# Kernel optimization log

Hardware: AMD Instinct MI355X
Metric: run time of the kernel (lower is better)

Reference implementation:

```python
import jax, jax.numpy as jnp
import numpy as np

CUTOFF = 5.0
L_MAX = 3
N_MAX = 3
DEGREE = L_MAX * N_MAX
EPS = 1e-8
NUM_NODES = 50000
NUM_EDGES = 1000000
NUM_TRIPLETS = 8000000
F_NODE = 64
F_EDGE = 64

# spherical Bessel zeros z_{l,n} for l<3, n<3
SB_ZEROS = np.array([
    [3.141592653589793, 6.283185307179586, 9.42477796076938],
    [4.4934094579080615, 7.725251836938652, 10.904121659429897],
    [5.763459196895549, 9.09501133047736, 12.322940970567323],
], dtype=np.float32)


def cutoff_function(r, cutoff):
    ratio = r / cutoff
    return 1 - 6 * ratio**5 + 15 * ratio**4 - 10 * ratio**3


def legendre_all(x, l_max):
    # P_0..P_{l_max-1}(x), x = cos(angle); returns list of arrays like x
    out = [jnp.ones_like(x)]
    if l_max >= 2:
        out.append(x)
        for n in range(1, l_max - 1):
            out.append(((2 * n + 1) * x * out[n] - n * out[n - 1]) / (n + 1))
    return out


def spherical_bessel(x, order):
    # j_order(x) via upward recurrence, matching the torch small-x branches
    safe = jnp.where(x > EPS, x, 1.0)
    out = [jnp.where(x > EPS, jnp.sin(x) / safe, jnp.ones_like(x))]
    if order >= 1:
        out.append(jnp.where(x > EPS, (jnp.sin(x) / safe - jnp.cos(x)) / safe, x / 3))
        coeff = 3
        for n in range(1, order):
            coeff *= 2 * n + 3
            out.append(jnp.where(x > EPS, (2 * n + 1) / safe * out[n] - out[n - 1], x / coeff))
    return out[-1]


def setup_inputs() -> dict:
    key = jax.random.key(0)
    ks = jax.random.split(key, 12)
    edge_distances = jax.random.uniform(ks[0], (NUM_EDGES,), minval=0.5, maxval=CUTOFF, dtype=jnp.float32)
    triplet_angles = jax.random.uniform(ks[1], (NUM_TRIPLETS,), minval=-1.0, maxval=1.0, dtype=jnp.float32)  # cos values
    node_features = jax.random.normal(ks[2], (NUM_NODES, F_NODE), dtype=jnp.float32)
    edge_attr = jax.random.normal(ks[3], (NUM_EDGES, F_EDGE), dtype=jnp.float32)
    triplet_edge_index = jax.random.randint(ks[4], (2, NUM_TRIPLETS), 0, NUM_EDGES)
    edge_index = jax.random.randint(ks[5], (2, NUM_EDGES), 0, NUM_NODES)
    s1 = 1.0 / np.sqrt(F_NODE)
    W1 = jax.random.uniform(ks[6], (F_NODE, DEGREE), minval=-s1, maxval=s1, dtype=jnp.float32)
    b1 = jax.random.uniform(ks[7], (DEGREE,), minval=-s1, maxval=s1, dtype=jnp.float32)
    s2 = 1.0 / np.sqrt(DEGREE)
    Wm = jax.random.uniform(ks[8], (DEGREE, F_EDGE), minval=-s2, maxval=s2, dtype=jnp.float32)
    bm = jax.random.uniform(ks[9], (F_EDGE,), minval=-s2, maxval=s2, dtype=jnp.float32)
    Wg = jax.random.uniform(ks[10], (DEGREE, F_EDGE), minval=-s2, maxval=s2, dtype=jnp.float32)
    bg = jax.random.uniform(ks[11], (F_EDGE,), minval=-s2, maxval=s2, dtype=jnp.float32)
    return {
        'edge_distances': edge_distances, 'triplet_angles': triplet_angles,
        'node_features': node_features, 'edge_attr': edge_attr,
        'W1': W1, 'b1': b1, 'Wm': Wm, 'bm': bm, 'Wg': Wg, 'bg': bg,
        'triplet_edge_index': triplet_edge_index, 'edge_index': edge_index,
    }


def reference(edge_distances, triplet_angles, node_features, edge_attr,
              W1, b1, Wm, bm, Wg, bg, triplet_edge_index, edge_index):
    tij, tik = triplet_edge_index[0], triplet_edge_index[1]
    rij = edge_distances[tij]                      # [T]
    rik = edge_distances[tik]                      # [T]
    fc = cutoff_function(rij, CUTOFF) * cutoff_function(rik, CUTOFF)  # [T]

    # angular basis: sqrt((2l+1)/pi) * P_l(cos theta), [L, T]
    leg = legendre_all(triplet_angles, L_MAX)
    sph = jnp.stack([np.sqrt((2 * l + 1) / np.pi).astype(np.float32) * leg[l]
                     for l in range(L_MAX)])

    # radial basis: j_l(z_{l,n} * r_ik / cutoff), [L, N_MAX, T]
    zeros = jnp.asarray(SB_ZEROS)
    jnlk = jnp.stack([
        spherical_bessel(zeros[l][:, None] * rik[None, :] / CUTOFF, l)
        for l in range(L_MAX)
    ])

    # node gate: sigmoid(Linear(node_features)) -> [L, N_MAX, num_nodes]
    m = jax.nn.sigmoid(node_features @ W1 + b1)    # [num_nodes, DEGREE]
    m = m.T.reshape(L_MAX, N_MAX, -1)
    node_k = edge_index[1][tik]                    # [T]

    tmp = jnlk * sph[:, None, :] * fc[None, None, :] * m[:, :, node_k]  # [L, N_MAX, T]

    # scatter-sum triplets -> edges: [num_edges, DEGREE]
    mid = jax.ops.segment_sum(tmp.reshape(DEGREE, -1).T, tij, num_segments=NUM_EDGES)

    # GatedMLP: swish main branch * sigmoid gate branch
    edge_update = jax.nn.silu(mid @ Wm + bm) * jax.nn.sigmoid(mid @ Wg + bg)
    return edge_attr + edge_update
```

## Files before the change

### kernel.cpp

```cpp
#include <hip/hip_runtime.h>
#include <hip/hip_fp16.h>
#include <math.h>

#define CUTOFF_INV 0.2f
#define EPB_SHIFT 10
#define EPB 1024
#define HEPB 512
#define NBIN_MAX 1024
#define P1_CHUNK 4096
#define P1_THREADS 1024
#define P2_THREADS 512
#define SCAP 5120
#define GC_STRIDE 16

typedef unsigned int uint;
typedef unsigned short ushort;

__device__ __forceinline__ float fcut(float r) {
    float p = r * CUTOFF_INV;
    float p2 = p * p;
    float p3 = p2 * p;
    return 1.0f + p3 * (-10.0f + p * (15.0f - 6.0f * p));
}

__device__ __forceinline__ void legendre_s(float ca, float& s0, float& s1, float& s2) {
    s0 = 0.5641895835477563f;
    s1 = 0.9772050238058398f * ca;
    s2 = 1.2615662610100802f * (1.5f * ca * ca - 0.5f);
}

__device__ __forceinline__ void radial9(float rik, float* v) {
    float rr = rik * CUTOFF_INV;
    float inv = __builtin_amdgcn_rcpf(rr);
    inv = inv * (2.0f - rr * inv);
    float fcik = fcut(rik);

    const float Z0[3]  = {3.14159265358979324f, 6.28318530717958648f, 9.42477796076937972f};
    const float IZ0[3] = {1.0f / 3.14159265358979324f, 1.0f / 6.28318530717958648f, 1.0f / 9.42477796076937972f};
    const float Z1[3]  = {4.49340945790806150f, 7.72525183693865170f, 10.9041216594298970f};
    const float IZ1[3] = {1.0f / 4.49340945790806150f, 1.0f / 7.72525183693865170f, 1.0f / 10.9041216594298970f};
    const float Z2[3]  = {5.76345919689554900f, 9.09501133047736000f, 12.3229409705673230f};
    const float IZ2[3] = {1.0f / 5.76345919689554900f, 1.0f / 9.09501133047736000f, 1.0f / 12.3229409705673230f};

#pragma unroll
    for (int n = 0; n < 3; ++n) {
        float x = Z0[n] * rr;
        float invx = IZ0[n] * inv;
        v[n] = __sinf(x) * invx * fcik;
    }
#pragma unroll
    for (int n = 0; n < 3; ++n) {
        float x = Z1[n] * rr;
        float invx = IZ1[n] * inv;
        float s, c;
        __sincosf(x, &s, &c);
        v[3 + n] = (s * invx - c) * invx * fcik;
    }
#pragma unroll
    for (int n = 0; n < 3; ++n) {
        float x = Z2[n] * rr;
        float invx = IZ2[n] * inv;
        float s, c;
        __sincosf(x, &s, &c);
        float sx = s * invx;
        float j1 = (sx - c) * invx;
        v[6 + n] = (3.0f * invx * j1 - sx) * fcik;
    }
}

__device__ __forceinline__ float h2f(uint w) { return __half2float(__ushort_as_half((ushort)w)); }

__device__ __forceinline__ void contrib9(uint2 r, const uint* __restrict__ gate16h, float* c) {
    uint nk = r.y & 0xFFFFu;
    const uint* G = gate16h + ((size_t)nk << 3);
    uint4 q = *(const uint4*)G;
    uint q8 = G[4];
    float ca  = h2f(r.x >> 16);
    float rik = h2f(r.x & 0xFFFFu);
    float vr[9];
    radial9(rik, vr);
    float s0, s1, s2;
    legendre_s(ca, s0, s1, s2);
    c[0] = vr[0] * h2f(q.x & 0xFFFFu) * s0;
    c[1] = vr[1] * h2f(q.x >> 16) * s0;
    c[2] = vr[2] * h2f(q.y & 0xFFFFu) * s0;
    c[3] = vr[3] * h2f(q.y >> 16) * s1;
    c[4] = vr[4] * h2f(q.z & 0xFFFFu) * s1;
    c[5] = vr[5] * h2f(q.z >> 16) * s1;
    c[6] = vr[6] * h2f(q.w & 0xFFFFu) * s2;
    c[7] = vr[7] * h2f(q.w >> 16) * s2;
    c[8] = vr[8] * h2f(q8 & 0xFFFFu) * s2;
}

__global__ void node_gate_h16_kernel(const float* __restrict__ nf,
                                     const float* __restrict__ W1,
                                     const float* __restrict__ b1,
                                     uint* __restrict__ gate16h, int N) {
    __shared__ float sW[64 * 9];
    __shared__ float sb[9];
    for (int i = threadIdx.x; i < 576; i += blockDim.x) sW[i] = W1[i];
    if (threadIdx.x < 9) sb[threadIdx.x] = b1[threadIdx.x];
    __syncthreads();
    int t = blockIdx.x * blockDim.x + threadIdx.x;
    if (t >= N) return;
    float acc[9];
#pragma unroll
    for (int d = 0; d < 9; ++d) acc[d] = sb[d];
    const float* row = nf + (size_t)t * 64;
#pragma unroll
    for (int f = 0; f < 64; ++f) {
        float x = row[f];
#pragma unroll
        for (int d = 0; d < 9; ++d) acc[d] += x * sW[f * 9 + d];
    }
    float g[9];
#pragma unroll
    for (int d = 0; d < 9; ++d) g[d] = 1.0f / (1.0f + __expf(-acc[d]));
    uint* o = gate16h + ((size_t)t << 3);
#pragma unroll
    for (int d = 0; d < 4; ++d) {
        uint lo = (uint)__half_as_ushort(__float2half_rn(g[2 * d]));
        uint hi = (uint)__half_as_ushort(__float2half_rn(g[2 * d + 1]));
        o[d] = lo | (hi << 16);
    }
    o[4] = (uint)__half_as_ushort(__float2half_rn(g[8]));
    o[5] = 0u; o[6] = 0u; o[7] = 0u;
}

__global__ void node_gate_f32_kernel(const float* __restrict__ nf,
                                     const float* __restrict__ W1,
                                     const float* __restrict__ b1,
                                     float* __restrict__ gate, int N) {
    __shared__ float sW[64 * 9];
    __shared__ float sb[9];
    for (int i = threadIdx.x; i < 576; i += blockDim.x) sW[i] = W1[i];
    if (threadIdx.x < 9) sb[threadIdx.x] = b1[threadIdx.x];
    __syncthreads();
    int t = blockIdx.x * blockDim.x + threadIdx.x;
    if (t >= N) return;
    float acc[9];
#pragma unroll
    for (int d = 0; d < 9; ++d) acc[d] = sb[d];
    const float* row = nf + (size_t)t * 64;
#pragma unroll
    for (int f = 0; f < 64; ++f) {
        float x = row[f];
#pragma unroll
        for (int d = 0; d < 9; ++d) acc[d] += x * sW[f * 9 + d];
    }
#pragma unroll
    for (int d = 0; d < 9; ++d)
        gate[(size_t)t * 9 + d] = 1.0f / (1.0f + __expf(-acc[d]));
}

__global__ void edge_tab_kernel(const float* __restrict__ dist,
                                const int* __restrict__ eidx,
                                uint* __restrict__ tab, int E) {
    int e = blockIdx.x * blockDim.x + threadIdx.x;
    if (e >= E) return;
    uint rh = (uint)__half_as_ushort(__float2half_rn(dist[e]));
    tab[e] = (rh << 16) | (uint)eidx[E + e];
}

__device__ __forceinline__ void spill_rec(uint2 rec, int bin,
                                          const uint* __restrict__ gate16h,
                                          float* __restrict__ mid) {
    float c[9];
    contrib9(rec, gate16h, c);
    uint ijl = rec.y >> 16;
    float* dst = mid + ((size_t)bin * EPB + ijl) * 9;
#pragma unroll
    for (int d = 0; d < 9; ++d) atomicAdd(dst + d, c[d]);
}

__global__ void __launch_bounds__(P1_THREADS) p1_sort_kernel(
        const float* __restrict__ ang,
        const int* __restrict__ tidx,
        const uint* __restrict__ tab,
        uint* __restrict__ gcount,
        uint2* __restrict__ binbuf,
        const uint* __restrict__ gate16h,
        float* __restrict__ mid,
        int T, int NBIN, int BCAP) {
    __shared__ uint hist[NBIN_MAX];
    __shared__ uint sc[NBIN_MAX];
    __shared__ uint gbase[NBIN_MAX];
    __shared__ uint lcur[NBIN_MAX];
    __shared__ uint2 sbuf[P1_CHUNK];
    __shared__ ushort sbin[P1_CHUNK];

    int t0 = blockIdx.x * P1_CHUNK;
    int m = T - t0;
    if (m <= 0) return;
    if (m > P1_CHUNK) m = P1_CHUNK;
    int tid = threadIdx.x;

    for (int i = tid; i < NBIN; i += blockDim.x) { hist[i] = 0; lcur[i] = 0; }
    __syncthreads();

    for (int i = tid; i < m; i += blockDim.x)
        atomicAdd(&hist[((uint)tidx[t0 + i]) >> EPB_SHIFT], 1u);
    __syncthreads();

    if (tid < NBIN) sc[tid] = hist[tid];
    __syncthreads();
    for (int off = 1; off < NBIN; off <<= 1) {
        uint v = 0;
        if (tid < NBIN) {
            v = sc[tid];
            if (tid >= off) v += sc[tid - off];
        }
        __syncthreads();
        if (tid < NBIN) sc[tid] = v;
        __syncthreads();
    }
    uint ex = 0, h = 0;
    if (tid < NBIN) {
        h = hist[tid];
        ex = sc[tid] - h;
    }
    __syncthreads();
    if (tid < NBIN) {
        sc[tid] = ex;
        gbase[tid] = h ? atomicAdd(&gcount[tid * GC_STRIDE], h) : 0u;
    }
    __syncthreads();

    for (int i = tid; i < m; i += blockDim.x) {
        int t = t0 + i;
        uint ij = (uint)tidx[t];
        uint ik = (uint)tidx[T + t];
        float ca = ang[t];
        uint te = tab[ik];
        uint bin = ij >> EPB_SHIFT;
        uint loc = atomicAdd(&lcur[bin], 1u);
        uint p = sc[bin] + loc;
        uint cah = (uint)__half_as_ushort(__float2half_rn(ca));
        sbuf[p] = make_uint2((cah << 16) | (te >> 16),
                             ((ij & (EPB - 1u)) << 16) | (te & 0xFFFFu));
        sbin[p] = (ushort)bin;
    }
    __syncthreads();

    for (int i = tid; i < m; i += blockDim.x) {
        uint bin = sbin[i];
        uint2 rec = sbuf[i];
        uint slot = gbase[bin] + ((uint)i - sc[bin]);
        if (slot < (uint)BCAP) {
            binbuf[(size_t)bin * BCAP + slot] = rec;
        } else {
            atomicOr(&gcount[bin * GC_STRIDE + 1], 1u);
            spill_rec(rec, bin, gate16h, mid);
        }
    }
}

__global__ void __launch_bounds__(P2_THREADS) p2_sorted_kernel(
        const float* __restrict__ dist,
        const uint* __restrict__ gate16h,
        const uint* __restrict__ gcount,
        const uint2* __restrict__ binbuf,
        const float* __restrict__ mid,
        const float* __restrict__ attr,
        const float* __restrict__ Wm,
        const float* __restrict__ bm,
        const float* __restrict__ Wg,
        const float* __restrict__ bg,
        float* __restrict__ out,
        int E, int BCAP) {
    __shared__ uint2 srec[SCAP];
    __shared__ uint cnt[HEPB];
    __shared__ uint off[HEPB];
    __shared__ float sWm[576], sWg[576], sbm[64], sbg[64];
    float* umid = (float*)srec;

    int tid = threadIdx.x;
    for (int i = tid; i < 576; i += P2_THREADS) { sWm[i] = Wm[i]; sWg[i] = Wg[i]; }
    if (tid < 64) { sbm[tid] = bm[tid]; sbg[tid] = bg[tid]; }
    cnt[tid] = 0;

    int bin = blockIdx.x >> 1;
    int hh  = blockIdx.x & 1;
    int ebase = (bin << EPB_SHIFT) + hh * HEPB;
    int ecnt = E - ebase; if (ecnt < 0) ecnt = 0; if (ecnt > HEPB) ecnt = HEPB;

    uint n = gcount[bin * GC_STRIDE];
    uint has_spill = gcount[bin * GC_STRIDE + 1];
    if (n > (uint)BCAP) n = (uint)BCAP;
    const uint2* rb = binbuf + (size_t)bin * BCAP;
    __syncthreads();

    for (uint i = tid; i < n; i += P2_THREADS) {
        uint ijl = rb[i].y >> 16;
        if ((ijl >> 9) == (uint)hh) atomicAdd(&cnt[ijl & (HEPB - 1u)], 1u);
    }
    __syncthreads();
    uint myCnt = cnt[tid];
    off[tid] = myCnt;
    __syncthreads();
    for (int o = 1; o < HEPB; o <<= 1) {
        uint add = (tid >= o) ? off[tid - o] : 0u;
        __syncthreads();
        off[tid] += add;
        __syncthreads();
    }
    uint total = off[HEPB - 1];
    uint myBase = off[tid] - myCnt;
    __syncthreads();
    off[tid] = myBase;
    cnt[tid] = 0;
    __syncthreads();

    float acc[9];
#pragma unroll
    for (int d = 0; d < 9; ++d) acc[d] = 0.0f;

    if (total <= (uint)SCAP) {
        for (uint i = tid; i < n; i += P2_THREADS) {
            uint2 r = rb[i];
            uint ijl = r.y >> 16;
            if ((ijl >> 9) == (uint)hh) {
                uint e = ijl & (HEPB - 1u);
                uint p = off[e] + atomicAdd(&cnt[e], 1u);
                srec[p] = r;
            }
        }
        __syncthreads();
        for (uint j = 0; j < myCnt; ++j) {
            float c[9];
            contrib9(srec[myBase + j], gate16h, c);
#pragma unroll
            for (int d = 0; d < 9; ++d) acc[d] += c[d];
        }
        __syncthreads();
    } else {
        for (int i = tid; i < HEPB * 9; i += P2_THREADS) umid[i] = 0.0f;
        __syncthreads();
        for (uint i = tid; i < n; i += P2_THREADS) {
            uint2 r = rb[i];
            uint ijl = r.y >> 16;
            if ((ijl >> 9) == (uint)hh) {
                uint e = ijl & (HEPB - 1u);
                float c[9];
                contrib9(r, gate16h, c);
                float* d0 = &umid[e * 9];
#pragma unroll
                for (int d = 0; d < 9; ++d) atomicAdd(d0 + d, c[d]);
            }
        }
        __syncthreads();
        if (tid < ecnt) {
#pragma unroll
            for (int d = 0; d < 9; ++d) acc[d] = umid[tid * 9 + d];
        }
        __syncthreads();
    }

    if (tid < ecnt) {
        int e = ebase + tid;
        float fc = fcut(dist[e]);
        if (has_spill) {
            const float* mg = mid + (size_t)e * 9;
#pragma unroll
            for (int d = 0; d < 9; ++d) acc[d] = fc * (acc[d] + mg[d]);
        } else {
#pragma unroll
            for (int d = 0; d < 9; ++d) acc[d] *= fc;
        }
#pragma unroll
        for (int d = 0; d < 9; ++d) umid[tid * 9 + d] = acc[d];
    }
    __syncthreads();

    int wid  = tid >> 6;
    int lane = tid & 63;
    for (int el = wid; el < ecnt; el += (P2_THREADS >> 6)) {
        int e = ebase + el;
        const float* ls = &umid[el * 9];
        float am = sbm[lane], ag = sbg[lane];
#pragma unroll
        for (int d = 0; d < 9; ++d) {
            float ud = ls[d];
            am += ud * sWm[d * 64 + lane];
            ag += ud * sWg[d * 64 + lane];
        }
        float hsw = am / (1.0f + __expf(-am));
        float gt  = 1.0f / (1.0f + __expf(-ag));
        size_t ofs = (size_t)e * 64 + lane;
        out[ofs] = attr[ofs] + hsw * gt;
    }
}

__global__ void triplet_kernel(const float* __restrict__ dist,
                               const float* __restrict__ ang,
                               const int* __restrict__ tidx,
                               const int* __restrict__ eidx,
                               const float* __restrict__ gate,
                               float* __restrict__ mid,
                               int T, int E) {
    int t = blockIdx.x * blockDim.x + threadIdx.x;
    if (t >= T) return;
    int ij = tidx[t];
    int ik = tidx[T + t];
    float ca  = ang[t];
    float rij = dist[ij];
    float rik = dist[ik];
    float frij = fcut(rij);
    int nk = eidx[E + ik];
    const float* g = gate + (size_t)nk * 9;
    float vr[9];
    radial9(rik, vr);
    float s0, s1, s2;
    legendre_s(ca, s0, s1, s2);
    s0 *= frij; s1 *= frij; s2 *= frij;
    float* dst = mid + (size_t)ij * 9;
    atomicAdd(dst + 0, vr[0] * s0 * g[0]);
    atomicAdd(dst + 1, vr[1] * s0 * g[1]);
    atomicAdd(dst + 2, vr[2] * s0 * g[2]);
    atomicAdd(dst + 3, vr[3] * s1 * g[3]);
    atomicAdd(dst + 4, vr[4] * s1 * g[4]);
    atomicAdd(dst + 5, vr[5] * s1 * g[5]);
    atomicAdd(dst + 6, vr[6] * s2 * g[6]);
    atomicAdd(dst + 7, vr[7] * s2 * g[7]);
    atomicAdd(dst + 8, vr[8] * s2 * g[8]);
}

__global__ void edge_kernel(const float* __restrict__ mid,
                            const float* __restrict__ attr,
                            const float* __restrict__ Wm, const float* __restrict__ bm,
                            const float* __restrict__ Wg, const float* __restrict__ bg,
                            float* __restrict__ out, int E) {
    __shared__ float sWm[9 * 64], sWg[9 * 64], sbm[64], sbg[64];
    for (int i = threadIdx.x; i < 576; i += blockDim.x) {
        sWm[i] = Wm[i];
        sWg[i] = Wg[i];
    }
    if (threadIdx.x < 64) {
        sbm[threadIdx.x] = bm[threadIdx.x];
        sbg[threadIdx.x] = bg[threadIdx.x];
    }
    __syncthreads();
    int wid  = threadIdx.x >> 6;
    int lane = threadIdx.x & 63;
    int e = blockIdx.x * (blockDim.x >> 6) + wid;
    if (e >= E) return;
    const float* u = mid + (size_t)e * 9;
    float am = sbm[lane], ag = sbg[lane];
#pragma unroll
    for (int d = 0; d < 9; ++d) {
        float ud = u[d];
        am += ud * sWm[d * 64 + lane];
        ag += ud * sWg[d * 64 + lane];
    }
    float h  = am / (1.0f + __expf(-am));
    float gt = 1.0f / (1.0f + __expf(-ag));
    size_t off = (size_t)e * 64 + lane;
    out[off] = attr[off] + h * gt;
}

extern "C" void kernel_launch(void* const* d_in, const int* in_sizes, int n_in,
                              void* d_out, int out_size, void* d_ws, size_t ws_size,
                              hipStream_t stream) {
    const float* dist = (const float*)d_in[0];
    const float* ang  = (const float*)d_in[1];
    const float* nf   = (const float*)d_in[2];
    const float* attr = (const float*)d_in[3];
    const float* W1   = (const float*)d_in[4];
    const float* b1   = (const float*)d_in[5];
    const float* Wm   = (const float*)d_in[6];
    const float* bm   = (const float*)d_in[7];
    const float* Wg   = (const float*)d_in[8];
    const float* bg   = (const float*)d_in[9];
    const int* tidx   = (const int*)d_in[10];
    const int* eidx   = (const int*)d_in[11];

    int E = in_sizes[0];
    int T = in_sizes[1];
    int N = in_sizes[2] / 64;

    int NBIN = (E + EPB - 1) >> EPB_SHIFT;
    int mean = T / (NBIN > 0 ? NBIN : 1);

    int bcap1 = ((mean + mean / 8 + 512) + 15) & ~15;
    int bcap2 = ((mean + mean / 32 + 256) + 15) & ~15;

    size_t o_gate  = 0;
    size_t o_tab   = o_gate + (size_t)N * 8;
    size_t o_mid   = o_tab + (size_t)E;
    size_t o_gcnt  = o_mid + (size_t)E * 9;
    size_t o_bb    = (o_gcnt + (size_t)NBIN * GC_STRIDE + 15) & ~(size_t)15;
    auto need = [&](int cap) { return (o_bb + (size_t)NBIN * cap * 2) * 4; };

    int BCAP = 0;
    if (ws_size >= need(bcap1)) BCAP = bcap1;
    else if (ws_size >= need(bcap2)) BCAP = bcap2;

    bool newpath = (E <= (1 << 20)) && (N <= 65535) && (NBIN <= NBIN_MAX)
                   && (NBIN <= P1_THREADS) && (BCAP > 0);

    float* wsf = (float*)d_ws;

    if (newpath) {
        uint*  gate16h = (uint*)(wsf + o_gate);
        uint*  tab     = (uint*)(wsf + o_tab);
        float* mid     = wsf + o_mid;
        uint*  gcount  = (uint*)(wsf + o_gcnt);
        uint2* binbuf  = (uint2*)(wsf + o_bb);

        hipMemsetAsync(gcount, 0, (size_t)NBIN * GC_STRIDE * sizeof(uint), stream);
        hipMemsetAsync(mid, 0, (size_t)E * 9 * sizeof(float), stream);
        node_gate_h16_kernel<<<(N + 255) / 256, 256, 0, stream>>>(nf, W1, b1, gate16h, N);
        edge_tab_kernel<<<(E + 255) / 256, 256, 0, stream>>>(dist, eidx, tab, E);

        int p1grid = (T + P1_CHUNK - 1) / P1_CHUNK;
        p1_sort_kernel<<<p1grid, P1_THREADS, 0, stream>>>(ang, tidx, tab, gcount, binbuf,
                                                          gate16h, mid, T, NBIN, BCAP);
        p2_sorted_kernel<<<NBIN * 2, P2_THREADS, 0, stream>>>(dist, gate16h, gcount, binbuf, mid,
                                                              attr, Wm, bm, Wg, bg,
                                                              (float*)d_out, E, BCAP);
    } else {
        float* gate = wsf;
        float* mid = gate + (((size_t)N * 9 + 15) & ~(size_t)15);
        hipMemsetAsync(mid, 0, (size_t)E * 9 * sizeof(float), stream);
        node_gate_f32_kernel<<<(N + 255) / 256, 256, 0, stream>>>(nf, W1, b1, gate, N);
        triplet_kernel<<<(T + 255) / 256, 256, 0, stream>>>(dist, ang, tidx, eidx, gate, mid, T, E);
        edge_kernel<<<(E + 3) / 4, 256, 0, stream>>>(mid, attr, Wm, bm, Wg, bg, (float*)d_out, E);
    }
}
```

Before: 448.9 us.

## Split shared triplet records into padded SoA arrays and unroll gather loop by four

Stores the sorted per-edge triplet records as two separate padded uint arrays (one pad word per 16) instead of an array of uint2, so per-thread sequential reads hit different LDS banks. The scatter reuses the scanned cnt array as the running offset, which removes the separate off array. The accumulation loop is unrolled by four with all gate loads issued before the math, so more global gathers are in flight at once. Shared capacity (SCAP) shrinks, so more bins take the slower atomic fallback path, and the unrolled loop raises register pressure.

```diff
diff --git a/kernel.cpp b/kernel.cpp
--- a/kernel.cpp
+++ b/kernel.cpp
@@ -10,7 +10,9 @@
 #define P1_CHUNK 4096
 #define P1_THREADS 1024
 #define P2_THREADS 512
-#define SCAP 5120
+#define SCAP 4608
+#define SCAP_P 4896
+#define PHYS(p) ((p) + ((p) >> 4))
 #define GC_STRIDE 16
 
 typedef unsigned int uint;
@@ -268,11 +270,11 @@
         const float* __restrict__ bg,
         float* __restrict__ out,
         int E, int BCAP) {
-    __shared__ uint2 srec[SCAP];
+    __shared__ uint sx[SCAP_P];
+    __shared__ uint sy[SCAP_P];
     __shared__ uint cnt[HEPB];
-    __shared__ uint off[HEPB];
     __shared__ float sWm[576], sWg[576], sbm[64], sbg[64];
-    float* umid = (float*)srec;
+    float* umid = (float*)sx;
 
     int tid = threadIdx.x;
     for (int i = tid; i < 576; i += P2_THREADS) { sWm[i] = Wm[i]; sWg[i] = Wg[i]; }
@@ -296,24 +298,40 @@
     }
     __syncthreads();
     uint myCnt = cnt[tid];
-    off[tid] = myCnt;
-    __syncthreads();
     for (int o = 1; o < HEPB; o <<= 1) {
-        uint add = (tid >= o) ? off[tid - o] : 0u;
-        __syncthreads();
-        off[tid] += add;
-        __syncthreads();
-    }
-    uint total = off[HEPB - 1];
-    uint myBase = off[tid] - myCnt;
-    __syncthreads();
-    off[tid] = myBase;
-    cnt[tid] = 0;
+        uint add = (tid >= o) ? cnt[tid - o] : 0u;
+        __syncthreads();
+        cnt[tid] += add;
+        __syncthreads();
+    }
+    uint total = cnt[HEPB - 1];
+    uint myBase = cnt[tid] - myCnt;
+    __syncthreads();
+    cnt[tid] = myBase;
     __syncthreads();
 
     float acc[9];
 #pragma unroll
     for (int d = 0; d < 9; ++d) acc[d] = 0.0f;
+
+#define ACC_G(rx_, q_, q8_)                                           \
+    {                                                                 \
+        float ca  = h2f(rx_ >> 16);                                   \
+        float rik = h2f(rx_ & 0xFFFFu);                                \
+        float vr[9];                                                  \
+        radial9(rik, vr);                                             \
+        float s0, s1, s2;                                             \
+        legendre_s(ca, s0, s1, s2);                                   \
+        acc[0] += vr[0] * h2f(q_.x & 0xFFFFu) * s0;                   \
+        acc[1] += vr[1] * h2f(q_.x >> 16) * s0;                       \
+        acc[2] += vr[2] * h2f(q_.y & 0xFFFFu) * s0;                   \
+        acc[3] += vr[3] * h2f(q_.y >> 16) * s1;                       \
+        acc[4] += vr[4] * h2f(q_.z & 0xFFFFu) * s1;                   \
+        acc[5] += vr[5] * h2f(q_.z >> 16) * s1;                       \
+        acc[6] += vr[6] * h2f(q_.w & 0xFFFFu) * s2;                   \
+        acc[7] += vr[7] * h2f(q_.w >> 16) * s2;                       \
+        acc[8] += vr[8] * h2f(q8_ & 0xFFFFu) * s2;                    \
+    }
 
     if (total <= (uint)SCAP) {
         for (uint i = tid; i < n; i += P2_THREADS) {
@@ -321,16 +339,42 @@
             uint ijl = r.y >> 16;
             if ((ijl >> 9) == (uint)hh) {
                 uint e = ijl & (HEPB - 1u);
-                uint p = off[e] + atomicAdd(&cnt[e], 1u);
-                srec[p] = r;
+                uint p = atomicAdd(&cnt[e], 1u);
+                uint pp = PHYS(p);
+                sx[pp] = r.x;
+                sy[pp] = r.y;
             }
         }
         __syncthreads();
-        for (uint j = 0; j < myCnt; ++j) {
-            float c[9];
-            contrib9(srec[myBase + j], gate16h, c);
-#pragma unroll
-            for (int d = 0; d < 9; ++d) acc[d] += c[d];
+        uint j = 0;
+        for (; j + 4 <= myCnt; j += 4) {
+            uint p0 = PHYS(myBase + j);
+            uint p1 = PHYS(myBase + j + 1);
+            uint p2 = PHYS(myBase + j + 2);
+            uint p3 = PHYS(myBase + j + 3);
+            uint rx0 = sx[p0], ry0 = sy[p0];
+            uint rx1 = sx[p1], ry1 = sy[p1];
+            uint rx2 = sx[p2], ry2 = sy[p2];
+            uint rx3 = sx[p3], ry3 = sy[p3];
+            const uint* G0 = gate16h + ((size_t)(ry0 & 0xFFFFu) << 3);
+            const uint* G1 = gate16h + ((size_t)(ry1 & 0xFFFFu) << 3);
+            const uint* G2 = gate16h + ((size_t)(ry2 & 0xFFFFu) << 3);
+            const uint* G3 = gate16h + ((size_t)(ry3 & 0xFFFFu) << 3);
+            uint4 q0 = *(const uint4*)G0; uint q08 = G0[4];
+            uint4 q1 = *(const uint4*)G1; uint q18 = G1[4];
+            uint4 q2 = *(const uint4*)G2; uint q28 = G2[4];
+            uint4 q3 = *(const uint4*)G3; uint q38 = G3[4];
+            ACC_G(rx0, q0, q08)
+            ACC_G(rx1, q1, q18)
+            ACC_G(rx2, q2, q28)
+            ACC_G(rx3, q3, q38)
+        }
+        for (; j < myCnt; ++j) {
+            uint pp = PHYS(myBase + j);
+            uint rx = sx[pp], ry = sy[pp];
+            const uint* G = gate16h + ((size_t)(ry & 0xFFFFu) << 3);
+            uint4 q = *(const uint4*)G; uint q8 = G[4];
+            ACC_G(rx, q, q8)
         }
         __syncthreads();
     } else {
@@ -355,6 +399,7 @@
         }
         __syncthreads();
     }
+#undef ACC_G
 
     if (tid < ecnt) {
         int e = ebase + tid;
```

After: 619.7 us. 1.38x slower.

## Balance sorted triplet accumulation by splitting records evenly across threads

Applied to the files above, without the earlier changes.

In the sorted path each thread used to walk only the records of its own edge, so work per thread followed the uneven per-edge triplet counts. Now each thread takes an equal contiguous slice of the sorted records, accumulates runs that share an edge in registers, and flushes each run to a shared-memory per-edge buffer with atomic adds. This evens out the load across threads at the cost of a separate umid shared array (more LDS per block, which may lower occupancy) and some atomic flushes at run boundaries.

```diff
diff --git a/kernel.cpp b/kernel.cpp
--- a/kernel.cpp
+++ b/kernel.cpp
@@ -269,15 +269,16 @@
         float* __restrict__ out,
         int E, int BCAP) {
     __shared__ uint2 srec[SCAP];
+    __shared__ float umid[HEPB * 9];
     __shared__ uint cnt[HEPB];
     __shared__ uint off[HEPB];
     __shared__ float sWm[576], sWg[576], sbm[64], sbg[64];
-    float* umid = (float*)srec;
 
     int tid = threadIdx.x;
     for (int i = tid; i < 576; i += P2_THREADS) { sWm[i] = Wm[i]; sWg[i] = Wg[i]; }
     if (tid < 64) { sbm[tid] = bm[tid]; sbg[tid] = bg[tid]; }
     cnt[tid] = 0;
+    for (int i = tid; i < HEPB * 9; i += P2_THREADS) umid[i] = 0.0f;
 
     int bin = blockIdx.x >> 1;
     int hh  = blockIdx.x & 1;
@@ -310,10 +311,6 @@
     off[tid] = myBase;
     cnt[tid] = 0;
     __syncthreads();
-
-    float acc[9];
-#pragma unroll
-    for (int d = 0; d < 9; ++d) acc[d] = 0.0f;
 
     if (total <= (uint)SCAP) {
         for (uint i = tid; i < n; i += P2_THREADS) {
@@ -326,16 +323,39 @@
             }
         }
         __syncthreads();
-        for (uint j = 0; j < myCnt; ++j) {
+        uint K = (total + P2_THREADS - 1) / P2_THREADS;
+        K |= 1u;
+        uint jb = (uint)tid * K;
+        uint je = jb + K; if (je > total) je = total;
+        int cur = -1;
+        float acc[9];
+#pragma unroll
+        for (int d = 0; d < 9; ++d) acc[d] = 0.0f;
+        for (uint j = jb; j < je; ++j) {
+            uint2 r = srec[j];
+            int e = (int)((r.y >> 16) & (HEPB - 1u));
+            if (e != cur) {
+                if (cur >= 0) {
+                    float* d0 = &umid[cur * 9];
+#pragma unroll
+                    for (int d = 0; d < 9; ++d) atomicAdd(d0 + d, acc[d]);
+                }
+                cur = e;
+#pragma unroll
+                for (int d = 0; d < 9; ++d) acc[d] = 0.0f;
+            }
             float c[9];
-            contrib9(srec[myBase + j], gate16h, c);
+            contrib9(r, gate16h, c);
 #pragma unroll
             for (int d = 0; d < 9; ++d) acc[d] += c[d];
         }
+        if (cur >= 0) {
+            float* d0 = &umid[cur * 9];
+#pragma unroll
+            for (int d = 0; d < 9; ++d) atomicAdd(d0 + d, acc[d]);
+        }
         __syncthreads();
     } else {
-        for (int i = tid; i < HEPB * 9; i += P2_THREADS) umid[i] = 0.0f;
-        __syncthreads();
         for (uint i = tid; i < n; i += P2_THREADS) {
             uint2 r = rb[i];
             uint ijl = r.y >> 16;
@@ -349,26 +369,20 @@
             }
         }
         __syncthreads();
-        if (tid < ecnt) {
-#pragma unroll
-            for (int d = 0; d < 9; ++d) acc[d] = umid[tid * 9 + d];
-        }
-        __syncthreads();
     }
 
     if (tid < ecnt) {
         int e = ebase + tid;
         float fc = fcut(dist[e]);
+        float* ls = &umid[tid * 9];
         if (has_spill) {
             const float* mg = mid + (size_t)e * 9;
 #pragma unroll
-            for (int d = 0; d < 9; ++d) acc[d] = fc * (acc[d] + mg[d]);
+            for (int d = 0; d < 9; ++d) ls[d] = fc * (ls[d] + mg[d]);
         } else {
 #pragma unroll
-            for (int d = 0; d < 9; ++d) acc[d] *= fc;
-        }
-#pragma unroll
-        for (int d = 0; d < 9; ++d) umid[tid * 9 + d] = acc[d];
+            for (int d = 0; d < 9; ++d) ls[d] *= fc;
+        }
     }
     __syncthreads();
 
```

After: 531.0 us. 1.18x slower.

## Halve edge bins to 512 edges so each phase-2 block reads only its own bin

Applied to the files above, without the earlier changes.

Bins now cover 512 edges instead of 1024, so each phase-2 block owns a whole bin. Previously two blocks each read a 1024-edge bin and kept only their half, so every record was read twice. Phase 1 now handles up to 2048 bins by having each thread scan two bin counts, and it folds the local and global offsets into a single per-bin delta, which drops some shared arrays and barriers. The cost is twice as many global atomics on bin counters in phase 1 and more, smaller bins with relatively more capacity padding.

```diff
diff --git a/kernel.cpp b/kernel.cpp
--- a/kernel.cpp
+++ b/kernel.cpp
@@ -3,14 +3,13 @@
 #include <math.h>
 
 #define CUTOFF_INV 0.2f
-#define EPB_SHIFT 10
-#define EPB 1024
-#define HEPB 512
-#define NBIN_MAX 1024
+#define EPB_SHIFT 9
+#define EPB 512
+#define NBIN_MAX 2048
 #define P1_CHUNK 4096
 #define P1_THREADS 1024
 #define P2_THREADS 512
-#define SCAP 5120
+#define SCAP 4608
 #define GC_STRIDE 16
 
 typedef unsigned int uint;
@@ -167,7 +166,7 @@
                                           float* __restrict__ mid) {
     float c[9];
     contrib9(rec, gate16h, c);
-    uint ijl = rec.y >> 16;
+    uint ijl = (rec.y >> 16) & (EPB - 1u);
     float* dst = mid + ((size_t)bin * EPB + ijl) * 9;
 #pragma unroll
     for (int d = 0; d < 9; ++d) atomicAdd(dst + d, c[d]);
@@ -182,12 +181,12 @@
         const uint* __restrict__ gate16h,
         float* __restrict__ mid,
         int T, int NBIN, int BCAP) {
-    __shared__ uint hist[NBIN_MAX];
-    __shared__ uint sc[NBIN_MAX];
-    __shared__ uint gbase[NBIN_MAX];
+    __shared__ int  delta[NBIN_MAX];
     __shared__ uint lcur[NBIN_MAX];
+    __shared__ uint pairs[P1_THREADS];
     __shared__ uint2 sbuf[P1_CHUNK];
     __shared__ ushort sbin[P1_CHUNK];
+    uint* hist = (uint*)delta;
 
     int t0 = blockIdx.x * P1_CHUNK;
     int m = T - t0;
@@ -195,34 +194,37 @@
     if (m > P1_CHUNK) m = P1_CHUNK;
     int tid = threadIdx.x;
 
-    for (int i = tid; i < NBIN; i += blockDim.x) { hist[i] = 0; lcur[i] = 0; }
+    for (int i = tid; i < NBIN; i += blockDim.x) hist[i] = 0u;
     __syncthreads();
 
     for (int i = tid; i < m; i += blockDim.x)
         atomicAdd(&hist[((uint)tidx[t0 + i]) >> EPB_SHIFT], 1u);
     __syncthreads();
 
-    if (tid < NBIN) sc[tid] = hist[tid];
-    __syncthreads();
-    for (int off = 1; off < NBIN; off <<= 1) {
-        uint v = 0;
-        if (tid < NBIN) {
-            v = sc[tid];
-            if (tid >= off) v += sc[tid - off];
-        }
-        __syncthreads();
-        if (tid < NBIN) sc[tid] = v;
-        __syncthreads();
-    }
-    uint ex = 0, h = 0;
-    if (tid < NBIN) {
-        h = hist[tid];
-        ex = sc[tid] - h;
-    }
-    __syncthreads();
-    if (tid < NBIN) {
-        sc[tid] = ex;
-        gbase[tid] = h ? atomicAdd(&gcount[tid * GC_STRIDE], h) : 0u;
+    int b0 = 2 * tid, b1 = 2 * tid + 1;
+    uint h0 = (b0 < NBIN) ? hist[b0] : 0u;
+    uint h1 = (b1 < NBIN) ? hist[b1] : 0u;
+    pairs[tid] = h0 + h1;
+    __syncthreads();
+    for (int off = 1; off < P1_THREADS; off <<= 1) {
+        uint v = pairs[tid];
+        if (tid >= off) v += pairs[tid - off];
+        __syncthreads();
+        pairs[tid] = v;
+        __syncthreads();
+    }
+    uint exPair = pairs[tid] - (h0 + h1);
+    uint ex0 = exPair, ex1 = exPair + h0;
+    __syncthreads();
+    if (b0 < NBIN) {
+        lcur[b0] = ex0;
+        uint gb = h0 ? atomicAdd(&gcount[b0 * GC_STRIDE], h0) : 0u;
+        delta[b0] = (int)gb - (int)ex0;
+    }
+    if (b1 < NBIN) {
+        lcur[b1] = ex1;
+        uint gb = h1 ? atomicAdd(&gcount[b1 * GC_STRIDE], h1) : 0u;
+        delta[b1] = (int)gb - (int)ex1;
     }
     __syncthreads();
 
@@ -233,8 +235,7 @@
         float ca = ang[t];
         uint te = tab[ik];
         uint bin = ij >> EPB_SHIFT;
-        uint loc = atomicAdd(&lcur[bin], 1u);
-        uint p = sc[bin] + loc;
+        uint p = atomicAdd(&lcur[bin], 1u);
         uint cah = (uint)__half_as_ushort(__float2half_rn(ca));
         sbuf[p] = make_uint2((cah << 16) | (te >> 16),
                              ((ij & (EPB - 1u)) << 16) | (te & 0xFFFFu));
@@ -245,12 +246,12 @@
     for (int i = tid; i < m; i += blockDim.x) {
         uint bin = sbin[i];
         uint2 rec = sbuf[i];
-        uint slot = gbase[bin] + ((uint)i - sc[bin]);
-        if (slot < (uint)BCAP) {
+        int slot = i + delta[bin];
+        if ((uint)slot < (uint)BCAP) {
             binbuf[(size_t)bin * BCAP + slot] = rec;
         } else {
             atomicOr(&gcount[bin * GC_STRIDE + 1], 1u);
-            spill_rec(rec, bin, gate16h, mid);
+            spill_rec(rec, (int)bin, gate16h, mid);
         }
     }
 }
@@ -269,8 +270,8 @@
         float* __restrict__ out,
         int E, int BCAP) {
     __shared__ uint2 srec[SCAP];
-    __shared__ uint cnt[HEPB];
-    __shared__ uint off[HEPB];
+    __shared__ uint cnt[EPB];
+    __shared__ uint off[EPB];
     __shared__ float sWm[576], sWg[576], sbm[64], sbg[64];
     float* umid = (float*)srec;
 
@@ -279,10 +280,9 @@
     if (tid < 64) { sbm[tid] = bm[tid]; sbg[tid] = bg[tid]; }
     cnt[tid] = 0;
 
-    int bin = blockIdx.x >> 1;
-    int hh  = blockIdx.x & 1;
-    int ebase = (bin << EPB_SHIFT) + hh * HEPB;
-    int ecnt = E - ebase; if (ecnt < 0) ecnt = 0; if (ecnt > HEPB) ecnt = HEPB;
+    int bin = blockIdx.x;
+    int ebase = bin << EPB_SHIFT;
+    int ecnt = E - ebase; if (ecnt < 0) ecnt = 0; if (ecnt > EPB) ecnt = EPB;
 
     uint n = gcount[bin * GC_STRIDE];
     uint has_spill = gcount[bin * GC_STRIDE + 1];
@@ -290,21 +290,18 @@
     const uint2* rb = binbuf + (size_t)bin * BCAP;
     __syncthreads();
 
-    for (uint i = tid; i < n; i += P2_THREADS) {
-        uint ijl = rb[i].y >> 16;
-        if ((ijl >> 9) == (uint)hh) atomicAdd(&cnt[ijl & (HEPB - 1u)], 1u);
-    }
+    for (uint i = tid; i < n; i += P2_THREADS)
+        atomicAdd(&cnt[(rb[i].y >> 16) & (EPB - 1u)], 1u);
     __syncthreads();
     uint myCnt = cnt[tid];
     off[tid] = myCnt;
     __syncthreads();
-    for (int o = 1; o < HEPB; o <<= 1) {
+    for (int o = 1; o < EPB; o <<= 1) {
         uint add = (tid >= o) ? off[tid - o] : 0u;
         __syncthreads();
         off[tid] += add;
         __syncthreads();
     }
-    uint total = off[HEPB - 1];
     uint myBase = off[tid] - myCnt;
     __syncthreads();
     off[tid] = myBase;
@@ -315,15 +312,12 @@
 #pragma unroll
     for (int d = 0; d < 9; ++d) acc[d] = 0.0f;
 
-    if (total <= (uint)SCAP) {
+    if (n <= (uint)SCAP) {
         for (uint i = tid; i < n; i += P2_THREADS) {
             uint2 r = rb[i];
-            uint ijl = r.y >> 16;
-            if ((ijl >> 9) == (uint)hh) {
-                uint e = ijl & (HEPB - 1u);
-                uint p = off[e] + atomicAdd(&cnt[e], 1u);
-                srec[p] = r;
-            }
+            uint e = (r.y >> 16) & (EPB - 1u);
+            uint p = off[e] + atomicAdd(&cnt[e], 1u);
+            srec[p] = r;
         }
         __syncthreads();
         for (uint j = 0; j < myCnt; ++j) {
@@ -334,19 +328,16 @@
         }
         __syncthreads();
     } else {
-        for (int i = tid; i < HEPB * 9; i += P2_THREADS) umid[i] = 0.0f;
+        for (int i = tid; i < EPB * 9; i += P2_THREADS) umid[i] = 0.0f;
         __syncthreads();
         for (uint i = tid; i < n; i += P2_THREADS) {
             uint2 r = rb[i];
-            uint ijl = r.y >> 16;
-            if ((ijl >> 9) == (uint)hh) {
-                uint e = ijl & (HEPB - 1u);
-                float c[9];
-                contrib9(r, gate16h, c);
-                float* d0 = &umid[e * 9];
-#pragma unroll
-                for (int d = 0; d < 9; ++d) atomicAdd(d0 + d, c[d]);
-            }
+            uint e = (r.y >> 16) & (EPB - 1u);
+            float c[9];
+            contrib9(r, gate16h, c);
+            float* d0 = &umid[e * 9];
+#pragma unroll
+            for (int d = 0; d < 9; ++d) atomicAdd(d0 + d, c[d]);
         }
         __syncthreads();
         if (tid < ecnt) {
@@ -496,7 +487,7 @@
     else if (ws_size >= need(bcap2)) BCAP = bcap2;
 
     bool newpath = (E <= (1 << 20)) && (N <= 65535) && (NBIN <= NBIN_MAX)
-                   && (NBIN <= P1_THREADS) && (BCAP > 0);
+                   && (NBIN <= 2 * P1_THREADS) && (BCAP > 0);
 
     float* wsf = (float*)d_ws;
 
@@ -515,9 +506,9 @@
         int p1grid = (T + P1_CHUNK - 1) / P1_CHUNK;
         p1_sort_kernel<<<p1grid, P1_THREADS, 0, stream>>>(ang, tidx, tab, gcount, binbuf,
                                                           gate16h, mid, T, NBIN, BCAP);
-        p2_sorted_kernel<<<NBIN * 2, P2_THREADS, 0, stream>>>(dist, gate16h, gcount, binbuf, mid,
-                                                              attr, Wm, bm, Wg, bg,
-                                                              (float*)d_out, E, BCAP);
+        p2_sorted_kernel<<<NBIN, P2_THREADS, 0, stream>>>(dist, gate16h, gcount, binbuf, mid,
+                                                          attr, Wm, bm, Wg, bg,
+                                                          (float*)d_out, E, BCAP);
     } else {
         float* gate = wsf;
         float* mid = gate + (((size_t)N * 9 + 15) & ~(size_t)15);
```

New measurement: 477.3 us. +6.3%, slower.
